# Kernel optimization log

Hardware: AMD Instinct MI355X
Metric: run time of the kernel (lower is better)

## Reference

```python
import jax, jax.numpy as jnp
import numpy as np

MARGIN = 0.1
NEG_INF = -1e30


def _l2norm(x):
    return x / jnp.linalg.norm(x, axis=1, keepdims=True)


def setup_inputs() -> dict:
    key = jax.random.key(0)
    ks = jax.random.split(key, 6)
    d, nNeg, Q = 128, 10, 32
    triplet_len = nNeg + 2
    n = Q * triplet_len            # 384
    m = 65536                      # XBM memory bank size
    V = 2048                       # image-id space
    P, Nn = 10, 25                 # pos / hard-neg list lengths per query
    inputs_col = _l2norm(jax.random.normal(ks[0], (n, d), dtype=jnp.float32))
    inputs_row = _l2norm(jax.random.normal(ks[1], (m, d), dtype=jnp.float32))
    targets_row = jax.random.randint(ks[2], (m,), 0, V, dtype=jnp.int64)
    qidxs = jnp.arange(Q, dtype=jnp.int64) + V  # unique query ids, disjoint from db ids
    targets_col = jax.random.randint(ks[3], (n,), 0, V, dtype=jnp.int64)
    targets_col = targets_col.at[jnp.arange(0, n, triplet_len)].set(qidxs)
    pidxs = jax.random.randint(ks[4], (Q, P), 0, V, dtype=jnp.int64)
    nnegs = jax.random.randint(ks[5], (Q, Nn), 0, V, dtype=jnp.int64)
    return {"inputs_col": inputs_col, "inputs_row": inputs_row,
            "targets_col": targets_col, "targets_row": targets_row,
            "qidxs": qidxs, "pidxs": pidxs, "nnegs": nnegs, "nNeg": nNeg}


def reference(inputs_col, inputs_row, targets_col, targets_row, qidxs, pidxs, nnegs, nNeg):
    n = inputs_col.shape[0]
    triplet_len = nNeg + 2
    query_list = jnp.arange(0, n, triplet_len)          # [Q]
    Q = query_list.shape[0]
    query_idx = targets_col[query_list]                 # [Q]

    sim_mat = inputs_col @ inputs_row.T                 # [n, m]
    sims = sim_mat[query_list]                          # [Q, m]

    # per-query lookup of pos / neg id lists (qidxs are unique)
    qidx_local = jnp.argmax(qidxs[None, :] == query_idx[:, None], axis=1)
    this_pidx = pidxs[qidx_local]                       # [Q, P]
    this_nneg = nnegs[qidx_local]                       # [Q, Nn]

    # from_batch handling (only possible when shapes match; here memory-bank case)
    if targets_col.shape[0] == targets_row.shape[0]:
        fb = jnp.all(targets_col == targets_row)
        trc = jnp.where(fb, targets_row.at[query_list].set(-1), targets_row)
    else:
        fb = None
        trc = targets_row

    # isin masks, vectorized across queries: [Q, m]
    pos_mask = jnp.any(targets_row[None, :, None] == this_pidx[:, None, :], axis=-1)
    neg_mask = ~jnp.any(trc[None, :, None] == this_nneg[:, None, :], axis=-1)
    if fb is not None:
        neg_mask = jnp.where(fb, neg_mask.at[:, query_list].set(False), neg_mask)

    # sort was only used to read the max -> masked max suffices
    pos_max = jnp.max(jnp.where(pos_mask, sims, NEG_INF), axis=1)   # [Q]
    neg_max = jnp.max(jnp.where(neg_mask, sims, NEG_INF), axis=1)   # [Q]

    pos_sel = pos_mask & (sims < neg_max[:, None] + MARGIN)
    neg_sel = neg_mask & (sims > jnp.maximum(0.4, pos_max)[:, None] - MARGIN)

    pos_cnt = jnp.sum(pos_sel, axis=1)
    neg_cnt = jnp.sum(neg_sel, axis=1)
    pos_loss = jnp.where(pos_cnt > 0,
                         jnp.sum(jnp.where(pos_sel, 1.0 - sims, 0.0), axis=1) / jnp.maximum(pos_cnt, 1),
                         0.0)
    neg_loss = jnp.where(neg_cnt > 0,
                         jnp.sum(jnp.where(neg_sel, sims, 0.0), axis=1) / jnp.maximum(neg_cnt, 1),
                         0.0)

    has_pos = jnp.any(pos_mask, axis=1)                 # whole block skipped if no positives
    loss = jnp.sum(jnp.where(has_pos, pos_loss + neg_loss, 0.0)) / Q
    return loss
```

## Files before the change

kernel.cpp:

```cpp
#include <hip/hip_runtime.h>

#define NEG_INF_F (-1e30f)
#define MARGIN_F 0.1f
#define TABN 4096
#define BR 128
#define NT 256

__device__ __forceinline__ unsigned fkey(float f) {
    unsigned b = __float_as_uint(f);
    return (b & 0x80000000u) ? ~b : (b | 0x80000000u);
}
__device__ __forceinline__ float fdec(unsigned k) {
    unsigned b = (k & 0x80000000u) ? (k ^ 0x80000000u) : ~k;
    return __uint_as_float(b);
}

__global__ __launch_bounds__(256) void setup_kernel(
    const float* __restrict__ inputs_col,
    const int* __restrict__ targets_col,
    const int* __restrict__ qidxs,
    const int* __restrict__ pidxs,
    const int* __restrict__ nnegs,
    unsigned* __restrict__ ptab,
    unsigned* __restrict__ ntab,
    float* __restrict__ qT,
    unsigned* __restrict__ qkeys,
    float* __restrict__ accums,
    unsigned* __restrict__ bar,
    int d, int Q, int P, int Nn, int triplet_len)
{
    __shared__ int qmap[32];
    const int tid = threadIdx.x;

    if (tid < Q) {
        int t = targets_col[tid * triplet_len];
        int l = 0;
        for (int i = Q - 1; i >= 0; --i) if (qidxs[i] == t) l = i;
        qmap[tid] = l;
    }
    for (int i = tid; i < TABN; i += 256) { ptab[i] = 0u; ntab[i] = 0u; }
    if (tid < 2 * Q) qkeys[tid] = fkey(NEG_INF_F);
    if (tid < 160) accums[tid] = 0.f;
    if (tid < 2) bar[tid] = 0u;
    __syncthreads();

    for (int i = tid; i < Q * P; i += 256) {
        int q = i / P, k = i - q * P;
        int id = pidxs[qmap[q] * P + k];
        if ((unsigned)id < TABN) atomicOr(&ptab[id], 1u << q);
    }
    for (int i = tid; i < Q * Nn; i += 256) {
        int q = i / Nn, k = i - q * Nn;
        int id = nnegs[qmap[q] * Nn + k];
        if ((unsigned)id < TABN) atomicOr(&ntab[id], 1u << q);
    }
    for (int i = tid; i < d * Q; i += 256) {
        int dd = i >> 5, q = i & 31;
        qT[i] = inputs_col[(size_t)(q * triplet_len) * d + dd];
    }
}

__device__ __forceinline__ void gsync(unsigned* cnt, unsigned nblk) {
    __syncthreads();
    if (threadIdx.x == 0) {
        __threadfence();
        atomicAdd(cnt, 1u);
        while (__hip_atomic_load(cnt, __ATOMIC_RELAXED, __HIP_MEMORY_SCOPE_AGENT) < nblk)
            __builtin_amdgcn_s_sleep(2);
        __threadfence();
    }
    __syncthreads();
}

__global__ __launch_bounds__(NT) void fused_kernel(
    const float* __restrict__ qT,
    const float* __restrict__ rows,
    const int* __restrict__ targets_row,
    const unsigned* __restrict__ ptab,
    const unsigned* __restrict__ ntab,
    unsigned* __restrict__ qkeys,
    float* __restrict__ accums,
    unsigned* __restrict__ bar,
    float* __restrict__ out,
    int m, int nb)
{
    __shared__ float qv[128][32];
    __shared__ unsigned spk[32], snk[32];
    __shared__ float sthr[2][32];
    __shared__ float wpart[4][32][5];
    __shared__ int islast;

    const int tid = threadIdx.x;
    const int bid = blockIdx.x;
    const int j0 = bid * BR;
    const int qg = tid & 7, q0 = qg * 4;
    const int rg = tid >> 3;
    const int r0 = j0 + rg * 4;

    for (int i = tid; i < 128 * 32; i += NT) ((float*)qv)[i] = qT[i];
    if (tid < 32) { spk[tid] = fkey(NEG_INF_F); snk[tid] = fkey(NEG_INF_F); }

    unsigned pb[4], nbr[4];
#pragma unroll
    for (int ri = 0; ri < 4; ++ri) {
        int t = targets_row[r0 + ri];
        if ((unsigned)t < TABN) { pb[ri] = ptab[t]; nbr[ri] = ~ntab[t]; }
        else                    { pb[ri] = 0u; nbr[ri] = ~0u; }
    }

    const float* base = rows + (size_t)r0 * 128;
    float4 b0[4], b1[4], b2[4], b3[4];

#define LOADB(B, K4) { _Pragma("unroll") \
    for (int ri = 0; ri < 4; ++ri) B[ri] = *(const float4*)(base + ri * 128 + (K4) * 4); }

#define STEP(B, K4) { _Pragma("unroll") \
    for (int dk = 0; dk < 4; ++dk) { \
        float4 qf = *(const float4*)&qv[(K4) * 4 + dk][q0]; \
        _Pragma("unroll") \
        for (int qi = 0; qi < 4; ++qi) { \
            float qq = ((const float*)&qf)[qi]; \
            _Pragma("unroll") \
            for (int ri = 0; ri < 4; ++ri) \
                acc[qi][ri] = fmaf(qq, ((const float*)&B[ri])[dk], acc[qi][ri]); \
        } } }

    LOADB(b0, 0) LOADB(b1, 1) LOADB(b2, 2)

    __syncthreads();

    float acc[4][4];
#pragma unroll
    for (int a = 0; a < 4; ++a)
#pragma unroll
        for (int b = 0; b < 4; ++b) acc[a][b] = 0.f;

    for (int k4 = 0; k4 < 32; k4 += 4) {
        if (k4 + 3 < 32) LOADB(b3, k4 + 3)
        STEP(b0, k4 + 0)
        if (k4 + 4 < 32) LOADB(b0, k4 + 4)
        STEP(b1, k4 + 1)
        if (k4 + 5 < 32) LOADB(b1, k4 + 5)
        STEP(b2, k4 + 2)
        if (k4 + 6 < 32) LOADB(b2, k4 + 6)
        STEP(b3, k4 + 3)
    }

#pragma unroll
    for (int qi = 0; qi < 4; ++qi) {
        const int q = q0 + qi;
        float pmax = NEG_INF_F, nmax = NEG_INF_F;
#pragma unroll
        for (int r = 0; r < 4; ++r) {
            if ((pb[r] >> q) & 1u)  pmax = fmaxf(pmax, acc[qi][r]);
            if ((nbr[r] >> q) & 1u) nmax = fmaxf(nmax, acc[qi][r]);
        }
#pragma unroll
        for (int off = 32; off >= 8; off >>= 1) {
            pmax = fmaxf(pmax, __shfl_down(pmax, off));
            nmax = fmaxf(nmax, __shfl_down(nmax, off));
        }
        if ((tid & 63) < 8) {
            atomicMax(&spk[q], fkey(pmax));
            atomicMax(&snk[q], fkey(nmax));
        }
    }
    __syncthreads();
    if (tid < 64) {
        int side = tid >> 5, q = tid & 31;
        atomicMax(&qkeys[q * 2 + side], side ? snk[q] : spk[q]);
    }

    gsync(&bar[0], (unsigned)nb);

    if (tid < 64) {
        int side = tid >> 5, q = tid & 31;
        sthr[side][q] = fdec(qkeys[q * 2 + side]);
    }
    __syncthreads();

    const int wave = tid >> 6, lane = tid & 63;
#pragma unroll
    for (int qi = 0; qi < 4; ++qi) {
        const int q = q0 + qi;
        const float posThr = sthr[1][q] + MARGIN_F;
        const float negThr = fmaxf(0.4f, sthr[0][q]) - MARGIN_F;
        float ps = 0.f, pc = 0.f, ns = 0.f, nc = 0.f, pmc = 0.f;
#pragma unroll
        for (int r = 0; r < 4; ++r) {
            float s = acc[qi][r];
            unsigned pm = (pb[r] >> q) & 1u;
            unsigned nm = (nbr[r] >> q) & 1u;
            pmc += (float)pm;
            if (pm && s < posThr) { ps += 1.f - s; pc += 1.f; }
            if (nm && s > negThr) { ns += s;       nc += 1.f; }
        }
#pragma unroll
        for (int off = 32; off >= 8; off >>= 1) {
            ps  += __shfl_down(ps, off);
            pc  += __shfl_down(pc, off);
            ns  += __shfl_down(ns, off);
            nc  += __shfl_down(nc, off);
            pmc += __shfl_down(pmc, off);
        }
        if (lane < 8) {
            wpart[wave][lane * 4 + qi][0] = ps;
            wpart[wave][lane * 4 + qi][1] = pc;
            wpart[wave][lane * 4 + qi][2] = ns;
            wpart[wave][lane * 4 + qi][3] = nc;
            wpart[wave][lane * 4 + qi][4] = pmc;
        }
    }
    __syncthreads();
    if (tid < 160) {
        float v = 0.f;
#pragma unroll
        for (int w = 0; w < 4; ++w) v += wpart[w][tid / 5][tid % 5];
        atomicAdd(&accums[tid], v);
    }

    __syncthreads();
    if (tid == 0) {
        __threadfence();
        unsigned old = atomicAdd(&bar[1], 1u);
        islast = (old == (unsigned)(nb - 1)) ? 1 : 0;
    }
    __syncthreads();
    if (islast) {
        if (tid == 0) __threadfence();
        __syncthreads();
        if (tid < 64) {
            float v = 0.f;
            if (tid < 32) {
                float psv = accums[tid * 5 + 0];
                float pcv = accums[tid * 5 + 1];
                float nsv = accums[tid * 5 + 2];
                float ncv = accums[tid * 5 + 3];
                float pmc = accums[tid * 5 + 4];
                float pl = (pcv > 0.f) ? psv / pcv : 0.f;
                float nl = (ncv > 0.f) ? nsv / ncv : 0.f;
                v = (pmc > 0.f) ? (pl + nl) : 0.f;
            }
#pragma unroll
            for (int off = 32; off; off >>= 1) v += __shfl_down(v, off);
            if (tid == 0) out[0] = v / 32.0f;
        }
    }
}

extern "C" void kernel_launch(void* const* d_in, const int* in_sizes, int n_in,
                              void* d_out, int out_size, void* d_ws, size_t ws_size,
                              hipStream_t stream)
{
    const float* inputs_col = (const float*)d_in[0];
    const float* inputs_row = (const float*)d_in[1];
    const int* targets_col  = (const int*)d_in[2];
    const int* targets_row  = (const int*)d_in[3];
    const int* qidxs        = (const int*)d_in[4];
    const int* pidxs        = (const int*)d_in[5];
    const int* nnegs        = (const int*)d_in[6];

    const int n  = in_sizes[2];
    int m        = in_sizes[3];
    const int Q  = in_sizes[4];
    const int P  = in_sizes[5] / Q;
    const int Nn = in_sizes[6] / Q;
    const int d  = in_sizes[0] / n;
    const int triplet_len = n / Q;

    int nb = (m + BR - 1) / BR;

    char* ws = (char*)d_ws;
    size_t off = 0;
    unsigned* ptab  = (unsigned*)(ws + off); off += (size_t)TABN * 4;
    unsigned* ntab  = (unsigned*)(ws + off); off += (size_t)TABN * 4;
    float* qT       = (float*)(ws + off);    off += (size_t)d * Q * 4;
    unsigned* qkeys = (unsigned*)(ws + off); off += (size_t)Q * 2 * 4;
    float* accums   = (float*)(ws + off);    off += (size_t)160 * 4;
    unsigned* bar   = (unsigned*)(ws + off); off += 2 * 4;
    float* out      = (float*)d_out;

    setup_kernel<<<1, 256, 0, stream>>>(inputs_col, targets_col, qidxs, pidxs, nnegs,
                                        ptab, ntab, qT, qkeys, accums, bar,
                                        d, Q, P, Nn, triplet_len);

    fused_kernel<<<nb, NT, 0, stream>>>(qT, inputs_row, targets_row, ptab, ntab,
                                        qkeys, accums, bar, out, m, nb);
}
```

Measured before the change: 165.6 us.

## Stage row tiles through transposed shared memory with split-K across half-waves

Rows per block drop from 128 to 64, doubling the grid, and launch bounds request four blocks per SM. Row data is now loaded coalesced into a double-buffered, transposed shared-memory tile, replacing per-thread strided float4 loads held in registers. Each wave splits the K dimension between its two half-waves and combines partial sums with a cross-lane xor shuffle, and row masks are staged in shared memory. This aims to improve global-load coalescing and occupancy, at the cost of extra barriers, more blocks joining the grid-wide spin barrier, and a shorter per-block reduction tree.

Result: slower. 244.2 us (+47.5%).

```diff
diff --git a/kernel.cpp b/kernel.cpp
--- a/kernel.cpp
+++ b/kernel.cpp
@@ -3,7 +3,7 @@
 #define NEG_INF_F (-1e30f)
 #define MARGIN_F 0.1f
 #define TABN 4096
-#define BR 128
+#define BR 64
 #define NT 256
 
 __device__ __forceinline__ unsigned fkey(float f) {
@@ -72,7 +72,7 @@
     __syncthreads();
 }
 
-__global__ __launch_bounds__(NT) void fused_kernel(
+__global__ __launch_bounds__(NT, 4) void fused_kernel(
     const float* __restrict__ qT,
     const float* __restrict__ rows,
     const int* __restrict__ targets_row,
@@ -85,66 +85,94 @@
     int m, int nb)
 {
     __shared__ float qv[128][32];
+    __shared__ float kt[2][16][68];
+    __shared__ unsigned pbm[BR], nbm[BR];
     __shared__ unsigned spk[32], snk[32];
     __shared__ float sthr[2][32];
     __shared__ float wpart[4][32][5];
     __shared__ int islast;
 
-    const int tid = threadIdx.x;
-    const int bid = blockIdx.x;
-    const int j0 = bid * BR;
-    const int qg = tid & 7, q0 = qg * 4;
-    const int rg = tid >> 3;
-    const int r0 = j0 + rg * 4;
-
-    for (int i = tid; i < 128 * 32; i += NT) ((float*)qv)[i] = qT[i];
+    const int tid  = threadIdx.x;
+    const int bid  = blockIdx.x;
+    const int j0   = bid * BR;
+    const int lane = tid & 63;
+    const int wave = tid >> 6;
+    const int kh   = lane >> 5;
+    const int rg   = (lane >> 3) & 3;
+    const int qg   = lane & 7;
+    const int q0   = qg * 4;
+    const int rloc = wave * 16 + rg * 4;
+
+    for (int i = tid; i < 128 * 32 / 4; i += NT)
+        ((float4*)qv)[i] = ((const float4*)qT)[i];
     if (tid < 32) { spk[tid] = fkey(NEG_INF_F); snk[tid] = fkey(NEG_INF_F); }
+    if (tid < BR) {
+        int j = j0 + tid;
+        unsigned pbv = 0u, nbv = 0u;
+        if (j < m) {
+            int t = targets_row[j];
+            if ((unsigned)t < TABN) { pbv = ptab[t]; nbv = ~ntab[t]; }
+            else                    { nbv = ~0u; }
+        }
+        pbm[tid] = pbv; nbm[tid] = nbv;
+    }
+
+    const int sr  = tid >> 2;
+    const int sk4 = tid & 3;
+    int jr = j0 + sr; if (jr >= m) jr = m - 1;
+    const float* gsrc = rows + (size_t)jr * 128 + sk4 * 4;
+
+    {
+        float4 v0 = *(const float4*)(gsrc);
+        kt[0][sk4 * 4 + 0][sr] = v0.x;
+        kt[0][sk4 * 4 + 1][sr] = v0.y;
+        kt[0][sk4 * 4 + 2][sr] = v0.z;
+        kt[0][sk4 * 4 + 3][sr] = v0.w;
+    }
+    float4 vnext = *(const float4*)(gsrc + 16);
+    __syncthreads();
+
+    float acc[4][4];
+#pragma unroll
+    for (int a = 0; a < 4; ++a)
+#pragma unroll
+        for (int b = 0; b < 4; ++b) acc[a][b] = 0.f;
+
+    for (int c = 0; c < 8; ++c) {
+        const int B = c & 1;
+#pragma unroll
+        for (int s = 0; s < 8; ++s) {
+            const int kl = kh * 8 + s;
+            float4 qf = *(const float4*)&qv[c * 16 + kl][q0];
+            float4 rf = *(const float4*)&kt[B][kl][rloc];
+            const float* qp = (const float*)&qf;
+            const float* rp = (const float*)&rf;
+#pragma unroll
+            for (int qi = 0; qi < 4; ++qi)
+#pragma unroll
+                for (int ri = 0; ri < 4; ++ri)
+                    acc[qi][ri] = fmaf(qp[qi], rp[ri], acc[qi][ri]);
+        }
+        if (c < 7) {
+            __syncthreads();
+            kt[B ^ 1][sk4 * 4 + 0][sr] = vnext.x;
+            kt[B ^ 1][sk4 * 4 + 1][sr] = vnext.y;
+            kt[B ^ 1][sk4 * 4 + 2][sr] = vnext.z;
+            kt[B ^ 1][sk4 * 4 + 3][sr] = vnext.w;
+            if (c < 6) vnext = *(const float4*)(gsrc + (c + 2) * 16);
+            __syncthreads();
+        }
+    }
+
+#pragma unroll
+    for (int qi = 0; qi < 4; ++qi)
+#pragma unroll
+        for (int ri = 0; ri < 4; ++ri)
+            acc[qi][ri] += __shfl_xor(acc[qi][ri], 32);
 
     unsigned pb[4], nbr[4];
 #pragma unroll
-    for (int ri = 0; ri < 4; ++ri) {
-        int t = targets_row[r0 + ri];
-        if ((unsigned)t < TABN) { pb[ri] = ptab[t]; nbr[ri] = ~ntab[t]; }
-        else                    { pb[ri] = 0u; nbr[ri] = ~0u; }
-    }
-
-    const float* base = rows + (size_t)r0 * 128;
-    float4 b0[4], b1[4], b2[4], b3[4];
-
-#define LOADB(B, K4) { _Pragma("unroll") \
-    for (int ri = 0; ri < 4; ++ri) B[ri] = *(const float4*)(base + ri * 128 + (K4) * 4); }
-
-#define STEP(B, K4) { _Pragma("unroll") \
-    for (int dk = 0; dk < 4; ++dk) { \
-        float4 qf = *(const float4*)&qv[(K4) * 4 + dk][q0]; \
-        _Pragma("unroll") \
-        for (int qi = 0; qi < 4; ++qi) { \
-            float qq = ((const float*)&qf)[qi]; \
-            _Pragma("unroll") \
-            for (int ri = 0; ri < 4; ++ri) \
-                acc[qi][ri] = fmaf(qq, ((const float*)&B[ri])[dk], acc[qi][ri]); \
-        } } }
-
-    LOADB(b0, 0) LOADB(b1, 1) LOADB(b2, 2)
-
-    __syncthreads();
-
-    float acc[4][4];
-#pragma unroll
-    for (int a = 0; a < 4; ++a)
-#pragma unroll
-        for (int b = 0; b < 4; ++b) acc[a][b] = 0.f;
-
-    for (int k4 = 0; k4 < 32; k4 += 4) {
-        if (k4 + 3 < 32) LOADB(b3, k4 + 3)
-        STEP(b0, k4 + 0)
-        if (k4 + 4 < 32) LOADB(b0, k4 + 4)
-        STEP(b1, k4 + 1)
-        if (k4 + 5 < 32) LOADB(b1, k4 + 5)
-        STEP(b2, k4 + 2)
-        if (k4 + 6 < 32) LOADB(b2, k4 + 6)
-        STEP(b3, k4 + 3)
-    }
+    for (int r = 0; r < 4; ++r) { pb[r] = pbm[rloc + r]; nbr[r] = nbm[rloc + r]; }
 
 #pragma unroll
     for (int qi = 0; qi < 4; ++qi) {
@@ -155,12 +183,11 @@
             if ((pb[r] >> q) & 1u)  pmax = fmaxf(pmax, acc[qi][r]);
             if ((nbr[r] >> q) & 1u) nmax = fmaxf(nmax, acc[qi][r]);
         }
-#pragma unroll
-        for (int off = 32; off >= 8; off >>= 1) {
-            pmax = fmaxf(pmax, __shfl_down(pmax, off));
-            nmax = fmaxf(nmax, __shfl_down(nmax, off));
-        }
-        if ((tid & 63) < 8) {
+        pmax = fmaxf(pmax, __shfl_down(pmax, 8));
+        pmax = fmaxf(pmax, __shfl_down(pmax, 16));
+        nmax = fmaxf(nmax, __shfl_down(nmax, 8));
+        nmax = fmaxf(nmax, __shfl_down(nmax, 16));
+        if (lane < 8) {
             atomicMax(&spk[q], fkey(pmax));
             atomicMax(&snk[q], fkey(nmax));
         }
@@ -179,7 +206,6 @@
     }
     __syncthreads();
 
-    const int wave = tid >> 6, lane = tid & 63;
 #pragma unroll
     for (int qi = 0; qi < 4; ++qi) {
         const int q = q0 + qi;
@@ -195,14 +221,11 @@
             if (pm && s < posThr) { ps += 1.f - s; pc += 1.f; }
             if (nm && s > negThr) { ns += s;       nc += 1.f; }
         }
-#pragma unroll
-        for (int off = 32; off >= 8; off >>= 1) {
-            ps  += __shfl_down(ps, off);
-            pc  += __shfl_down(pc, off);
-            ns  += __shfl_down(ns, off);
-            nc  += __shfl_down(nc, off);
-            pmc += __shfl_down(pmc, off);
-        }
+        ps  += __shfl_down(ps, 8);  ps  += __shfl_down(ps, 16);
+        pc  += __shfl_down(pc, 8);  pc  += __shfl_down(pc, 16);
+        ns  += __shfl_down(ns, 8);  ns  += __shfl_down(ns, 16);
+        nc  += __shfl_down(nc, 8);  nc  += __shfl_down(nc, 16);
+        pmc += __shfl_down(pmc, 8); pmc += __shfl_down(pmc, 16);
         if (lane < 8) {
             wpart[wave][lane * 4 + qi][0] = ps;
             wpart[wave][lane * 4 + qi][1] = pc;
```
